# Kernel optimization log

Hardware: AMD Instinct MI355X
Metric: run time of the kernel (lower is better)

The kernel has to match this reference:

```python
import jax, jax.numpy as jnp
import numpy as np
from jax import lax
from jax.scipy.special import logsumexp

N, M, B, T_MAX = 16, 64, 512, 4096


def setup_inputs() -> dict:
    key = jax.random.key(0)
    k1, k2, k3, k4, k5 = jax.random.split(key, 5)
    return {
        "x": jax.random.randint(k1, (B, T_MAX), 0, M),            # observation indices
        "T": jax.random.randint(k2, (B,), 1, T_MAX + 1),          # lengths in [1, T_max]
        "trans_logits": jax.random.normal(k3, (N, N), jnp.float32),
        "emiss_logits": jax.random.normal(k4, (N, M), jnp.float32),
        "prior_logits": jax.random.normal(k5, (N,), jnp.float32),
    }


def reference(x, T, trans_logits, emiss_logits, prior_logits):
    # Normalizations exactly as in the torch module
    log_A = jax.nn.log_softmax(trans_logits, axis=0)   # (N, N), columns normalized: A[i,k] = log p(i | k)
    log_E = jax.nn.log_softmax(emiss_logits, axis=1)   # (N, M)
    log_pi = jax.nn.log_softmax(prior_logits)          # (N,)

    # t = 0: log_alpha[b, i] = log_E[i, x[b,0]] + log_pi[i]
    alpha0 = log_E[:, x[:, 0]].T + log_pi              # (B, N)

    def step(alpha, x_t):
        # new[b, i] = log_E[i, x_t[b]] + logsumexp_k (log_A[i,k] + alpha[b,k])
        trans = logsumexp(log_A[None, :, :] + alpha[:, None, :], axis=2)  # (B, N)
        new = log_E[:, x_t].T + trans
        # carry full alpha; emit only per-step logsumexp to avoid (T,B,N) buffer
        return new, logsumexp(new, axis=1)

    ls0 = logsumexp(alpha0, axis=1)                    # (B,)
    _, ls_rest = lax.scan(step, alpha0, x[:, 1:].T)    # ls_rest: (T_max-1, B)
    log_sums = jnp.concatenate([ls0[None, :], ls_rest], axis=0)  # (T_max, B)

    # gather log p(x_{1..T_b}) at index T_b - 1 for each batch element
    log_probs = jnp.take_along_axis(log_sums.T, (T - 1)[:, None], axis=1)  # (B, 1)
    return jnp.exp(log_probs)


if __name__ == "__main__":
    out = reference(**setup_inputs())
    print(out.shape, out.dtype)
```

## Files before the change

### kernel.cpp

```cpp
#include <hip/hip_runtime.h>
#include <hip/hip_bf16.h>


#define NS    16
#define MOBS  64
#define SSH   5
#define NSEG  32

typedef float f32x4 __attribute__((ext_vector_type(4)));
typedef short s16x4 __attribute__((ext_vector_type(4)));

static __device__ __forceinline__ int imin(int a, int b){ return a < b ? a : b; }

static __device__ __forceinline__ unsigned short f2bf(float f){
  return __bfloat16_as_ushort(__float2bfloat16(f));
}
static __device__ __forceinline__ float b2f(unsigned short u){
  unsigned bits = ((unsigned)u) << 16;
  return __builtin_bit_cast(float, bits);
}

static __device__ __forceinline__ s16x4 pack_bf16x4(f32x4 C){
  unsigned r0, r1;
  asm("v_cvt_pk_bf16_f32 %0, %1, %2" : "=v"(r0) : "v"(C.x), "v"(C.y));
  asm("v_cvt_pk_bf16_f32 %0, %1, %2" : "=v"(r1) : "v"(C.z), "v"(C.w));
  uint2 pu; pu.x = r0; pu.y = r1;
  return __builtin_bit_cast(s16x4, pu);
}

#if __has_builtin(__builtin_amdgcn_mfma_f32_16x16x16bf16_1k)
static __device__ __forceinline__ f32x4 mfma16(s16x4 a, s16x4 b, f32x4 c){
  return __builtin_amdgcn_mfma_f32_16x16x16bf16_1k(a, b, c, 0, 0, 0);
}
#else
static __device__ __forceinline__ f32x4 mfma16(s16x4 a, s16x4 b, f32x4 c){
  f32x4 d;
  asm volatile("v_mfma_f32_16x16x16_bf16 %0, %1, %2, %3"
               : "=&v"(d) : "v"(a), "v"(b), "v"(c));
  return d;
}
#endif


__global__ void hmm_setup(const float* __restrict__ tl, const float* __restrict__ el,
                          const float* __restrict__ pl, float* __restrict__ ws,
                          unsigned short* __restrict__ g2)
{
  int m = blockIdx.x, t = threadIdx.x;
  __shared__ float Al[256];
  __shared__ float ev[16];
  if (t < 16){
    float mx = -3.0e38f;
    for (int i = 0; i < 16; ++i) mx = fmaxf(mx, tl[i*NS + t]);
    float sm = 0.f;
    for (int i = 0; i < 16; ++i) sm += expf(tl[i*NS + t] - mx);
    float inv = 1.f / sm;
    for (int i = 0; i < 16; ++i) Al[i*16 + t] = expf(tl[i*NS + t] - mx) * inv;
  } else if (t < 32){
    int i = t - 16;
    if (m < 64){
      float mx = -3.0e38f;
      for (int mm = 0; mm < MOBS; ++mm) mx = fmaxf(mx, el[i*MOBS + mm]);
      float sm = 0.f;
      for (int mm = 0; mm < MOBS; ++mm) sm += expf(el[i*MOBS + mm] - mx);
      float v = expf(el[i*MOBS + m] - mx) / sm;
      ev[i] = v;
      ws[m*16 + i] = v;
      g2[16640 + m*16 + i] = f2bf(v);
    } else ev[i] = 1.f;
  } else if (t < 48 && m == 64){
    int i = t - 32;
    float mx = -3.0e38f;
    for (int k = 0; k < 16; ++k) mx = fmaxf(mx, pl[k]);
    float sm = 0.f;
    for (int k = 0; k < 16; ++k) sm += expf(pl[k] - mx);
    ws[1024 + i] = expf(pl[i] - mx) / sm;
  }
  __syncthreads();
  int l = t >> 2, e = t & 3;
  int i = l & 15, col = ((l >> 4) << 2) + e;
  float acc;
  if (m == 64){
    acc = Al[i*16 + col];
  } else {
    acc = 0.f;
    #pragma unroll
    for (int k = 0; k < 16; ++k) acc += Al[i*16 + k] * ev[k] * Al[k*16 + col];
  }
  g2[(m*64 + l)*4 + e] = f2bf(acc);
}

template<bool MASK, bool REN>
static __device__ __forceinline__ void run_quad(
    int p0, int npair,
    const unsigned short* g2l, const unsigned short* etl,
    int lane4, int g4, int xp, s16x4& P, int& ce,
    s16x4 (&gf)[4], s16x4 (&ev)[4], s16x4 (&gfn)[4], s16x4 (&evn)[4])
{
  const f32x4 Z = {0.f, 0.f, 0.f, 0.f};
  #pragma unroll
  for (int p = 0; p < 4; ++p){
    int v = __builtin_amdgcn_readlane(xp, (p0 + 4 + p) & 63);
    gfn[p] = *(const s16x4*)&g2l[(v & 63)*256 + lane4];
    evn[p] = *(const s16x4*)&etl[((v >> 8) & 63)*16 + g4];

    f32x4 C = mfma16(gf[p], P, Z);
    C.x *= b2f((unsigned short)ev[p].x);
    C.y *= b2f((unsigned short)ev[p].y);
    C.z *= b2f((unsigned short)ev[p].z);
    C.w *= b2f((unsigned short)ev[p].w);

    bool commit = (!MASK) || (p0 + p < npair);
    if (REN && p == 3){
      float mm = fmaxf(fmaxf(C.x, C.y), fmaxf(C.z, C.w));
      mm = fmaxf(mm, __shfl_xor(mm, 16));
      mm = fmaxf(mm, __shfl_xor(mm, 32));
      int kk; (void)frexpf(mm, &kk);
      if (commit){
        C.x = ldexpf(C.x, -kk); C.y = ldexpf(C.y, -kk);
        C.z = ldexpf(C.z, -kk); C.w = ldexpf(C.w, -kk);
        ce += kk;
      }
    }
    if (commit){
      P = pack_bf16x4(C);
    }
    asm volatile("" ::: "memory");
  }
}

__global__ __launch_bounds__(512, 1) void hmm_seg(
    const int* __restrict__ x, const int* __restrict__ Tl,
    const unsigned short* __restrict__ g2,
    unsigned short* __restrict__ Q, int* __restrict__ CE,
    int TMAX, int XN)
{
  int tid  = threadIdx.x;
  int lane = tid & 63;
  int wid  = __builtin_amdgcn_readfirstlane(tid >> 6);
  int g = lane >> 4, j = lane & 15;
  int lane4 = lane * 4, g4 = g * 4;

  int gseg = blockIdx.x * 8 + wid;
  int b = gseg >> SSH, s = gseg & (NSEG - 1);

  int steps = __builtin_amdgcn_readfirstlane(Tl[b]) - 1;
  int L  = (steps + NSEG - 1) >> SSH;
  int lo = s * L;
  int n  = imin(steps - lo, L);

  unsigned short* Qout = Q + (size_t)gseg * 256;
  int* ceout = CE + gseg * NS;

  int s_lo = (blockIdx.x & 3) * 8;
  if (s_lo * L >= steps){
    if (g == 0) ceout[j] = 0;
    #pragma unroll
    for (int e = 0; e < 4; ++e){
      int k = 4*g + e;
      Qout[k*16 + j] = (k == j) ? (unsigned short)0x3F80 : (unsigned short)0;
    }
    return;
  }

  __shared__ unsigned short g2l[64*256];
  __shared__ unsigned short etl[1024];
  {
    const uint4* s1 = (const uint4*)g2;
    const uint4* s2 = (const uint4*)(g2 + 16640);
    uint4* d1 = (uint4*)g2l;
    uint4* d2 = (uint4*)etl;
    for (int i = tid; i < 2048; i += 512) d1[i] = s1[i];
    if (tid < 128) d2[tid] = s2[tid];
  }
  __syncthreads();

  if (n <= 0){
    if (g == 0) ceout[j] = 0;
    #pragma unroll
    for (int e = 0; e < 4; ++e){
      int k = 4*g + e;
      Qout[k*16 + j] = (k == j) ? (unsigned short)0x3F80 : (unsigned short)0;
    }
    return;
  }

  int npair = n >> 1, odd = n & 1;
  int xbase = b*TMAX + 1 + lo;

  int i0 = xbase + 2*lane;
  int xa = x[imin(i0,     XN - 1)] & 63;
  int xb = x[imin(i0 + 1, XN - 1)] & 63;
  int xp = xa | (xb << 8);

  s16x4 P;
  P.x = (4*g+0 == j) ? (short)0x3F80 : (short)0;
  P.y = (4*g+1 == j) ? (short)0x3F80 : (short)0;
  P.z = (4*g+2 == j) ? (short)0x3F80 : (short)0;
  P.w = (4*g+3 == j) ? (short)0x3F80 : (short)0;

  s16x4 gfA[4], gfB[4], evA[4], evB[4];
  #pragma unroll
  for (int p = 0; p < 4; ++p){
    int v = __builtin_amdgcn_readlane(xp, p);
    gfA[p] = *(const s16x4*)&g2l[(v & 63)*256 + lane4];
    evA[p] = *(const s16x4*)&etl[((v >> 8) & 63)*16 + g4];
  }

  int ce = 0, p0 = 0;
  while (p0 + 8 <= npair){
    run_quad<false,false>(p0,   npair, g2l, etl, lane4, g4, xp, P, ce, gfA, evA, gfB, evB);
    run_quad<false,true >(p0+4, npair, g2l, etl, lane4, g4, xp, P, ce, gfB, evB, gfA, evA);
    p0 += 8;
  }
  if (p0 < npair){
    run_quad<true,true>(p0, npair, g2l, etl, lane4, g4, xp, P, ce, gfA, evA, gfB, evB);
    if (p0 + 4 < npair)
      run_quad<true,true>(p0+4, npair, g2l, etl, lane4, g4, xp, P, ce, gfB, evB, gfA, evA);
  }

  if (odd){
    int v = __builtin_amdgcn_readlane(xp, (n - 1) >> 1);
    int xm = v & 63;
    s16x4 af  = *(const s16x4*)&g2[16384 + lane4];
    s16x4 evo = *(const s16x4*)&etl[xm*16 + g4];
    const f32x4 Z = {0.f,0.f,0.f,0.f};
    f32x4 C = mfma16(af, P, Z);
    C.x *= b2f((unsigned short)evo.x); C.y *= b2f((unsigned short)evo.y);
    C.z *= b2f((unsigned short)evo.z); C.w *= b2f((unsigned short)evo.w);
    P = pack_bf16x4(C);
  }

  if (g == 0) ceout[j] = ce;
  unsigned short pb[4] = {(unsigned short)P.x, (unsigned short)P.y,
                          (unsigned short)P.z, (unsigned short)P.w};
  #pragma unroll
  for (int e = 0; e < 4; ++e) Qout[(4*g + e)*16 + j] = pb[e];
}

__global__ __launch_bounds__(256) void hmm_comb(
    const int* __restrict__ x, const float* __restrict__ ws,
    const unsigned short* __restrict__ Q, const int* __restrict__ CE,
    float* __restrict__ out, int TMAX)
{
  int lane = threadIdx.x & 63;
  int w    = threadIdx.x >> 6;
  int b    = blockIdx.x * 4 + w;
  int k = lane & 15, r = lane >> 4;

  int x0 = x[b*TMAX];
  float u = ws[1024 + k] * ws[x0*16 + k];
  int ce_tot = 0;

  const unsigned short* qb = Q  + (size_t)b * NSEG * 256;
  const int*            cb = CE + b * NSEG * 16;

  s16x4 qq = *(const s16x4*)&qb[k*16 + 4*r];
  int4  cv = *(const int4*)&cb[4*r];

  for (int s = 0; s < NSEG; ++s){
    s16x4 qn; int4 cn;
    if (s + 1 < NSEG){
      qn = *(const s16x4*)&qb[(s+1)*256 + k*16 + 4*r];
      cn = *(const int4*)&cb[(s+1)*16 + 4*r];
    }
    int c0 = __builtin_amdgcn_readlane(cv.x, 0);
    float m0 = ldexpf(b2f((unsigned short)qq.x), cv.x - c0);
    float m1 = ldexpf(b2f((unsigned short)qq.y), cv.y - c0);
    float m2 = ldexpf(b2f((unsigned short)qq.z), cv.z - c0);
    float m3 = ldexpf(b2f((unsigned short)qq.w), cv.w - c0);

    float u0 = __shfl(u, 4*r + 0);
    float u1 = __shfl(u, 4*r + 1);
    float u2 = __shfl(u, 4*r + 2);
    float u3 = __shfl(u, 4*r + 3);
    float acc = m0*u0 + m1*u1 + m2*u2 + m3*u3;
    acc += __shfl_xor(acc, 16);
    acc += __shfl_xor(acc, 32);

    int ek; (void)frexpf(acc, &ek);
    int k0 = __builtin_amdgcn_readlane(ek, 0);
    u = ldexpf(acc, -k0);
    ce_tot += c0 + k0;

    qq = qn; cv = cn;
  }

  float sm = u;
  sm += __shfl_xor(sm, 1);
  sm += __shfl_xor(sm, 2);
  sm += __shfl_xor(sm, 4);
  sm += __shfl_xor(sm, 8);
  if (lane == 0) out[b] = ldexpf(sm, ce_tot);
}

extern "C" void kernel_launch(void* const* d_in, const int* in_sizes, int n_in,
                              void* d_out, int out_size, void* d_ws, size_t ws_size,
                              hipStream_t stream)
{
  (void)n_in; (void)out_size; (void)ws_size;
  const int*   x  = (const int*)  d_in[0];
  const int*   T  = (const int*)  d_in[1];
  const float* tl = (const float*)d_in[2];
  const float* el = (const float*)d_in[3];
  const float* pl = (const float*)d_in[4];
  int B    = in_sizes[1];
  int TMAX = in_sizes[0] / B;
  int XN   = B * TMAX;

  float* ws = (float*)d_ws;
  unsigned short* g2 = (unsigned short*)((char*)d_ws + 8192);
  unsigned short* Q  = (unsigned short*)((char*)d_ws + 49152);
  int* CE = (int*)((char*)d_ws + 49152 + (size_t)B * NSEG * 512);
  float* out = (float*)d_out;

  hipLaunchKernelGGL(hmm_setup, dim3(65),          dim3(256), 0, stream, tl, el, pl, ws, g2);
  hipLaunchKernelGGL(hmm_seg,   dim3(B*NSEG/8),    dim3(512), 0, stream, x, T, g2, Q, CE, TMAX, XN);
  hipLaunchKernelGGL(hmm_comb,  dim3(B/4),         dim3(256), 0, stream, x, ws, Q, CE, out, TMAX);
}
```

Measured before the change: 50.59 us.

## Split each segment into two interleaved MFMA chains and merge via matmul

Each wave now runs two independent matrix-product chains over the two halves of its segment, interleaving their MFMAs so the dependent latency of one chain hides behind the other. The second chain's product is transposed through a small LDS buffer and multiplied onto the first at the end, with one renormalization and a combined exponent. This adds register pressure, an extra LDS round-trip, an extra MFMA per segment, and a change in how bf16 rounding accumulates.

```diff
diff --git a/kernel.cpp b/kernel.cpp
--- a/kernel.cpp
+++ b/kernel.cpp
@@ -91,41 +91,74 @@
 }
 
 template<bool MASK, bool REN>
-static __device__ __forceinline__ void run_quad(
-    int p0, int npair,
+static __device__ __forceinline__ void run_quad2(
+    int p0, int h, int c2n,
     const unsigned short* g2l, const unsigned short* etl,
-    int lane4, int g4, int xp, s16x4& P, int& ce,
-    s16x4 (&gf)[4], s16x4 (&ev)[4], s16x4 (&gfn)[4], s16x4 (&evn)[4])
+    int lane4, int g4, int xp,
+    s16x4& P1, int& ce1,
+    s16x4 (&gf1)[4], s16x4 (&ev1)[4], s16x4 (&g1n)[4], s16x4 (&e1n)[4],
+    s16x4& P2, int& ce2,
+    s16x4 (&gf2)[4], s16x4 (&ev2)[4], s16x4 (&g2n)[4], s16x4 (&e2n)[4])
 {
   const f32x4 Z = {0.f, 0.f, 0.f, 0.f};
   #pragma unroll
   for (int p = 0; p < 4; ++p){
-    int v = __builtin_amdgcn_readlane(xp, (p0 + 4 + p) & 63);
-    gfn[p] = *(const s16x4*)&g2l[(v & 63)*256 + lane4];
-    evn[p] = *(const s16x4*)&etl[((v >> 8) & 63)*16 + g4];
-
-    f32x4 C = mfma16(gf[p], P, Z);
-    C.x *= b2f((unsigned short)ev[p].x);
-    C.y *= b2f((unsigned short)ev[p].y);
-    C.z *= b2f((unsigned short)ev[p].z);
-    C.w *= b2f((unsigned short)ev[p].w);
-
-    bool commit = (!MASK) || (p0 + p < npair);
-    if (REN && p == 3){
-      float mm = fmaxf(fmaxf(C.x, C.y), fmaxf(C.z, C.w));
-      mm = fmaxf(mm, __shfl_xor(mm, 16));
-      mm = fmaxf(mm, __shfl_xor(mm, 32));
-      int kk; (void)frexpf(mm, &kk);
-      if (commit){
-        C.x = ldexpf(C.x, -kk); C.y = ldexpf(C.y, -kk);
-        C.z = ldexpf(C.z, -kk); C.w = ldexpf(C.w, -kk);
-        ce += kk;
+    {
+      int v = __builtin_amdgcn_readlane(xp, (p0 + 4 + p) & 63);
+      g1n[p] = *(const s16x4*)&g2l[(v & 63)*256 + lane4];
+      e1n[p] = *(const s16x4*)&etl[((v >> 8) & 63)*16 + g4];
+
+      f32x4 C = mfma16(gf1[p], P1, Z);
+      C.x *= b2f((unsigned short)ev1[p].x);
+      C.y *= b2f((unsigned short)ev1[p].y);
+      C.z *= b2f((unsigned short)ev1[p].z);
+      C.w *= b2f((unsigned short)ev1[p].w);
+
+      bool commit = (!MASK) || (p0 + p < h);
+      if (REN && p == 3){
+        float mm = fmaxf(fmaxf(C.x, C.y), fmaxf(C.z, C.w));
+        mm = fmaxf(mm, __shfl_xor(mm, 16));
+        mm = fmaxf(mm, __shfl_xor(mm, 32));
+        int kk; (void)frexpf(mm, &kk);
+        if (commit){
+          C.x = ldexpf(C.x, -kk); C.y = ldexpf(C.y, -kk);
+          C.z = ldexpf(C.z, -kk); C.w = ldexpf(C.w, -kk);
+          ce1 += kk;
+        }
       }
-    }
-    if (commit){
-      P = pack_bf16x4(C);
-    }
-    asm volatile("" ::: "memory");
+      if (commit) P1 = pack_bf16x4(C);
+      asm volatile("" ::: "memory");
+    }
+    {
+      int v = __builtin_amdgcn_readlane(xp, (h + p0 + 4 + p) & 63);
+      g2n[p] = *(const s16x4*)&g2l[(v & 63)*256 + lane4];
+      e2n[p] = *(const s16x4*)&etl[((v >> 8) & 63)*16 + g4];
+
+      f32x4 D = mfma16(gf2[p], P2, Z);
+      D.x *= b2f((unsigned short)ev2[p].x);
+      D.y *= b2f((unsigned short)ev2[p].y);
+      D.z *= b2f((unsigned short)ev2[p].z);
+      D.w *= b2f((unsigned short)ev2[p].w);
+
+      bool commit = (!MASK) || (p0 + p < c2n);
+      if (REN && p == 3){
+        float mm = fmaxf(fmaxf(D.x, D.y), fmaxf(D.z, D.w));
+        mm = fmaxf(mm, __shfl_xor(mm, 1));
+        mm = fmaxf(mm, __shfl_xor(mm, 2));
+        mm = fmaxf(mm, __shfl_xor(mm, 4));
+        mm = fmaxf(mm, __shfl_xor(mm, 8));
+        mm = fmaxf(mm, __shfl_xor(mm, 16));
+        mm = fmaxf(mm, __shfl_xor(mm, 32));
+        int kk; (void)frexpf(mm, &kk);
+        if (commit){
+          D.x = ldexpf(D.x, -kk); D.y = ldexpf(D.y, -kk);
+          D.z = ldexpf(D.z, -kk); D.w = ldexpf(D.w, -kk);
+          ce2 += kk;
+        }
+      }
+      if (commit) P2 = pack_bf16x4(D);
+      asm volatile("" ::: "memory");
+    }
   }
 }
 
@@ -165,6 +198,7 @@
 
   __shared__ unsigned short g2l[64*256];
   __shared__ unsigned short etl[1024];
+  __shared__ unsigned short tb[2048];
   {
     const uint4* s1 = (const uint4*)g2;
     const uint4* s2 = (const uint4*)(g2 + 16640);
@@ -186,6 +220,8 @@
   }
 
   int npair = n >> 1, odd = n & 1;
+  int h   = npair >> 1;
+  int c2n = npair - h;
   int xbase = b*TMAX + 1 + lo;
 
   int i0 = xbase + 2*lane;
@@ -193,45 +229,82 @@
   int xb = x[imin(i0 + 1, XN - 1)] & 63;
   int xp = xa | (xb << 8);
 
-  s16x4 P;
-  P.x = (4*g+0 == j) ? (short)0x3F80 : (short)0;
-  P.y = (4*g+1 == j) ? (short)0x3F80 : (short)0;
-  P.z = (4*g+2 == j) ? (short)0x3F80 : (short)0;
-  P.w = (4*g+3 == j) ? (short)0x3F80 : (short)0;
-
-  s16x4 gfA[4], gfB[4], evA[4], evB[4];
+  s16x4 P1, P2;
+  P1.x = (4*g+0 == j) ? (short)0x3F80 : (short)0;
+  P1.y = (4*g+1 == j) ? (short)0x3F80 : (short)0;
+  P1.z = (4*g+2 == j) ? (short)0x3F80 : (short)0;
+  P1.w = (4*g+3 == j) ? (short)0x3F80 : (short)0;
+  P2 = P1;
+
+  s16x4 gf1A[4], gf1B[4], ev1A[4], ev1B[4];
+  s16x4 gf2A[4], gf2B[4], ev2A[4], ev2B[4];
   #pragma unroll
   for (int p = 0; p < 4; ++p){
-    int v = __builtin_amdgcn_readlane(xp, p);
-    gfA[p] = *(const s16x4*)&g2l[(v & 63)*256 + lane4];
-    evA[p] = *(const s16x4*)&etl[((v >> 8) & 63)*16 + g4];
-  }
-
-  int ce = 0, p0 = 0;
-  while (p0 + 8 <= npair){
-    run_quad<false,false>(p0,   npair, g2l, etl, lane4, g4, xp, P, ce, gfA, evA, gfB, evB);
-    run_quad<false,true >(p0+4, npair, g2l, etl, lane4, g4, xp, P, ce, gfB, evB, gfA, evA);
+    int v1 = __builtin_amdgcn_readlane(xp, p);
+    gf1A[p] = *(const s16x4*)&g2l[(v1 & 63)*256 + lane4];
+    ev1A[p] = *(const s16x4*)&etl[((v1 >> 8) & 63)*16 + g4];
+    int v2 = __builtin_amdgcn_readlane(xp, (h + p) & 63);
+    gf2A[p] = *(const s16x4*)&g2l[(v2 & 63)*256 + lane4];
+    ev2A[p] = *(const s16x4*)&etl[((v2 >> 8) & 63)*16 + g4];
+  }
+
+  int ce1 = 0, ce2 = 0, p0 = 0;
+  while (p0 + 8 <= h){
+    run_quad2<false,false>(p0,   h, c2n, g2l, etl, lane4, g4, xp,
+                           P1, ce1, gf1A, ev1A, gf1B, ev1B,
+                           P2, ce2, gf2A, ev2A, gf2B, ev2B);
+    run_quad2<false,true >(p0+4, h, c2n, g2l, etl, lane4, g4, xp,
+                           P1, ce1, gf1B, ev1B, gf1A, ev1A,
+                           P2, ce2, gf2B, ev2B, gf2A, ev2A);
     p0 += 8;
   }
-  if (p0 < npair){
-    run_quad<true,true>(p0, npair, g2l, etl, lane4, g4, xp, P, ce, gfA, evA, gfB, evB);
-    if (p0 + 4 < npair)
-      run_quad<true,true>(p0+4, npair, g2l, etl, lane4, g4, xp, P, ce, gfB, evB, gfA, evA);
-  }
+  if (p0 < c2n){
+    run_quad2<true,true>(p0, h, c2n, g2l, etl, lane4, g4, xp,
+                         P1, ce1, gf1A, ev1A, gf1B, ev1B,
+                         P2, ce2, gf2A, ev2A, gf2B, ev2B);
+    if (p0 + 4 < c2n)
+      run_quad2<true,true>(p0+4, h, c2n, g2l, etl, lane4, g4, xp,
+                           P1, ce1, gf1B, ev1B, gf1A, ev1A,
+                           P2, ce2, gf2B, ev2B, gf2A, ev2A);
+  }
+
+  s16x4 A2;
+  {
+    unsigned short* twave = tb + wid*256;
+    ((uint2*)twave)[lane] = __builtin_bit_cast(uint2, P2);
+    int base = (lane >> 4)*16 + ((lane & 15) >> 2)*64 + (lane & 3);
+    unsigned u0 = twave[base +  0];
+    unsigned u1 = twave[base +  4];
+    unsigned u2 = twave[base +  8];
+    unsigned u3 = twave[base + 12];
+    uint2 au; au.x = u0 | (u1 << 16); au.y = u2 | (u3 << 16);
+    A2 = __builtin_bit_cast(s16x4, au);
+  }
+  const f32x4 Z = {0.f,0.f,0.f,0.f};
+  f32x4 C = mfma16(A2, P1, Z);
+  {
+    float mm = fmaxf(fmaxf(C.x, C.y), fmaxf(C.z, C.w));
+    mm = fmaxf(mm, __shfl_xor(mm, 16));
+    mm = fmaxf(mm, __shfl_xor(mm, 32));
+    int kk; (void)frexpf(mm, &kk);
+    C.x = ldexpf(C.x, -kk); C.y = ldexpf(C.y, -kk);
+    C.z = ldexpf(C.z, -kk); C.w = ldexpf(C.w, -kk);
+    ce1 += ce2 + kk;
+  }
+  s16x4 P = pack_bf16x4(C);
 
   if (odd){
     int v = __builtin_amdgcn_readlane(xp, (n - 1) >> 1);
     int xm = v & 63;
     s16x4 af  = *(const s16x4*)&g2[16384 + lane4];
     s16x4 evo = *(const s16x4*)&etl[xm*16 + g4];
-    const f32x4 Z = {0.f,0.f,0.f,0.f};
-    f32x4 C = mfma16(af, P, Z);
-    C.x *= b2f((unsigned short)evo.x); C.y *= b2f((unsigned short)evo.y);
-    C.z *= b2f((unsigned short)evo.z); C.w *= b2f((unsigned short)evo.w);
-    P = pack_bf16x4(C);
-  }
-
-  if (g == 0) ceout[j] = ce;
+    f32x4 Co = mfma16(af, P, Z);
+    Co.x *= b2f((unsigned short)evo.x); Co.y *= b2f((unsigned short)evo.y);
+    Co.z *= b2f((unsigned short)evo.z); Co.w *= b2f((unsigned short)evo.w);
+    P = pack_bf16x4(Co);
+  }
+
+  if (g == 0) ceout[j] = ce1;
   unsigned short pb[4] = {(unsigned short)P.x, (unsigned short)P.y,
                           (unsigned short)P.z, (unsigned short)P.w};
   #pragma unroll
```

Result: slower. 57.03 us (+12.7%).

## Fuse segment-combine into segment kernel via last-block atomic counter

Applied to the files above, without the earlier changes.

Removes the separate combine kernel launch. Each of the 4 blocks serving a batch element bumps an atomic counter after finishing its segments, and the last block's first wave runs the sequential 32-segment combine and writes the output. The setup kernel zeroes the counters. This saves a launch and its gap, but adds threadfences, an atomic and a block-wide sync, and the combine now runs in a single wave inside the tail blocks.

```diff
diff --git a/kernel.cpp b/kernel.cpp
--- a/kernel.cpp
+++ b/kernel.cpp
@@ -44,11 +44,15 @@
 
 __global__ void hmm_setup(const float* __restrict__ tl, const float* __restrict__ el,
                           const float* __restrict__ pl, float* __restrict__ ws,
-                          unsigned short* __restrict__ g2)
+                          unsigned short* __restrict__ g2, int* __restrict__ cnt,
+                          int B)
 {
   int m = blockIdx.x, t = threadIdx.x;
   __shared__ float Al[256];
   __shared__ float ev[16];
+  if (m == 64){
+    for (int i = t; i < B; i += 256) cnt[i] = 0;
+  }
   if (t < 16){
     float mx = -3.0e38f;
     for (int i = 0; i < 16; ++i) mx = fmaxf(mx, tl[i*NS + t]);
@@ -131,10 +135,15 @@
 
 __global__ __launch_bounds__(512, 1) void hmm_seg(
     const int* __restrict__ x, const int* __restrict__ Tl,
+    const float* __restrict__ wsf,
     const unsigned short* __restrict__ g2,
     unsigned short* __restrict__ Q, int* __restrict__ CE,
+    int* __restrict__ cnt, float* __restrict__ out,
     int TMAX, int XN)
 {
+  __shared__ unsigned short g2l[64*256];
+  __shared__ unsigned short etl[1024];
+
   int tid  = threadIdx.x;
   int lane = tid & 63;
   int wid  = __builtin_amdgcn_readfirstlane(tid >> 6);
@@ -153,145 +162,145 @@
   int* ceout = CE + gseg * NS;
 
   int s_lo = (blockIdx.x & 3) * 8;
-  if (s_lo * L >= steps){
+  bool blk_empty = (s_lo * L >= steps);
+
+  if (blk_empty){
     if (g == 0) ceout[j] = 0;
     #pragma unroll
     for (int e = 0; e < 4; ++e){
       int k = 4*g + e;
       Qout[k*16 + j] = (k == j) ? (unsigned short)0x3F80 : (unsigned short)0;
     }
-    return;
-  }
-
-  __shared__ unsigned short g2l[64*256];
-  __shared__ unsigned short etl[1024];
-  {
-    const uint4* s1 = (const uint4*)g2;
-    const uint4* s2 = (const uint4*)(g2 + 16640);
-    uint4* d1 = (uint4*)g2l;
-    uint4* d2 = (uint4*)etl;
-    for (int i = tid; i < 2048; i += 512) d1[i] = s1[i];
-    if (tid < 128) d2[tid] = s2[tid];
-  }
+  } else {
+    {
+      const uint4* s1 = (const uint4*)g2;
+      const uint4* s2 = (const uint4*)(g2 + 16640);
+      uint4* d1 = (uint4*)g2l;
+      uint4* d2 = (uint4*)etl;
+      for (int i = tid; i < 2048; i += 512) d1[i] = s1[i];
+      if (tid < 128) d2[tid] = s2[tid];
+    }
+    __syncthreads();
+
+    if (n <= 0){
+      if (g == 0) ceout[j] = 0;
+      #pragma unroll
+      for (int e = 0; e < 4; ++e){
+        int k = 4*g + e;
+        Qout[k*16 + j] = (k == j) ? (unsigned short)0x3F80 : (unsigned short)0;
+      }
+    } else {
+      int npair = n >> 1, odd = n & 1;
+      int xbase = b*TMAX + 1 + lo;
+
+      int i0 = xbase + 2*lane;
+      int xa = x[imin(i0,     XN - 1)] & 63;
+      int xb = x[imin(i0 + 1, XN - 1)] & 63;
+      int xp = xa | (xb << 8);
+
+      s16x4 P;
+      P.x = (4*g+0 == j) ? (short)0x3F80 : (short)0;
+      P.y = (4*g+1 == j) ? (short)0x3F80 : (short)0;
+      P.z = (4*g+2 == j) ? (short)0x3F80 : (short)0;
+      P.w = (4*g+3 == j) ? (short)0x3F80 : (short)0;
+
+      s16x4 gfA[4], gfB[4], evA[4], evB[4];
+      #pragma unroll
+      for (int p = 0; p < 4; ++p){
+        int v = __builtin_amdgcn_readlane(xp, p);
+        gfA[p] = *(const s16x4*)&g2l[(v & 63)*256 + lane4];
+        evA[p] = *(const s16x4*)&etl[((v >> 8) & 63)*16 + g4];
+      }
+
+      int ce = 0, p0 = 0;
+      while (p0 + 8 <= npair){
+        run_quad<false,false>(p0,   npair, g2l, etl, lane4, g4, xp, P, ce, gfA, evA, gfB, evB);
+        run_quad<false,true >(p0+4, npair, g2l, etl, lane4, g4, xp, P, ce, gfB, evB, gfA, evA);
+        p0 += 8;
+      }
+      if (p0 < npair){
+        run_quad<true,true>(p0, npair, g2l, etl, lane4, g4, xp, P, ce, gfA, evA, gfB, evB);
+        if (p0 + 4 < npair)
+          run_quad<true,true>(p0+4, npair, g2l, etl, lane4, g4, xp, P, ce, gfB, evB, gfA, evA);
+      }
+
+      if (odd){
+        int v = __builtin_amdgcn_readlane(xp, (n - 1) >> 1);
+        int xm = v & 63;
+        s16x4 af  = *(const s16x4*)&g2[16384 + lane4];
+        s16x4 evo = *(const s16x4*)&etl[xm*16 + g4];
+        const f32x4 Z = {0.f,0.f,0.f,0.f};
+        f32x4 C = mfma16(af, P, Z);
+        C.x *= b2f((unsigned short)evo.x); C.y *= b2f((unsigned short)evo.y);
+        C.z *= b2f((unsigned short)evo.z); C.w *= b2f((unsigned short)evo.w);
+        P = pack_bf16x4(C);
+      }
+
+      if (g == 0) ceout[j] = ce;
+      unsigned short pb[4] = {(unsigned short)P.x, (unsigned short)P.y,
+                              (unsigned short)P.z, (unsigned short)P.w};
+      #pragma unroll
+      for (int e = 0; e < 4; ++e) Qout[(4*g + e)*16 + j] = pb[e];
+    }
+  }
+
   __syncthreads();
-
-  if (n <= 0){
-    if (g == 0) ceout[j] = 0;
-    #pragma unroll
-    for (int e = 0; e < 4; ++e){
-      int k = 4*g + e;
-      Qout[k*16 + j] = (k == j) ? (unsigned short)0x3F80 : (unsigned short)0;
-    }
-    return;
-  }
-
-  int npair = n >> 1, odd = n & 1;
-  int xbase = b*TMAX + 1 + lo;
-
-  int i0 = xbase + 2*lane;
-  int xa = x[imin(i0,     XN - 1)] & 63;
-  int xb = x[imin(i0 + 1, XN - 1)] & 63;
-  int xp = xa | (xb << 8);
-
-  s16x4 P;
-  P.x = (4*g+0 == j) ? (short)0x3F80 : (short)0;
-  P.y = (4*g+1 == j) ? (short)0x3F80 : (short)0;
-  P.z = (4*g+2 == j) ? (short)0x3F80 : (short)0;
-  P.w = (4*g+3 == j) ? (short)0x3F80 : (short)0;
-
-  s16x4 gfA[4], gfB[4], evA[4], evB[4];
-  #pragma unroll
-  for (int p = 0; p < 4; ++p){
-    int v = __builtin_amdgcn_readlane(xp, p);
-    gfA[p] = *(const s16x4*)&g2l[(v & 63)*256 + lane4];
-    evA[p] = *(const s16x4*)&etl[((v >> 8) & 63)*16 + g4];
-  }
-
-  int ce = 0, p0 = 0;
-  while (p0 + 8 <= npair){
-    run_quad<false,false>(p0,   npair, g2l, etl, lane4, g4, xp, P, ce, gfA, evA, gfB, evB);
-    run_quad<false,true >(p0+4, npair, g2l, etl, lane4, g4, xp, P, ce, gfB, evB, gfA, evA);
-    p0 += 8;
-  }
-  if (p0 < npair){
-    run_quad<true,true>(p0, npair, g2l, etl, lane4, g4, xp, P, ce, gfA, evA, gfB, evB);
-    if (p0 + 4 < npair)
-      run_quad<true,true>(p0+4, npair, g2l, etl, lane4, g4, xp, P, ce, gfB, evB, gfA, evA);
-  }
-
-  if (odd){
-    int v = __builtin_amdgcn_readlane(xp, (n - 1) >> 1);
-    int xm = v & 63;
-    s16x4 af  = *(const s16x4*)&g2[16384 + lane4];
-    s16x4 evo = *(const s16x4*)&etl[xm*16 + g4];
-    const f32x4 Z = {0.f,0.f,0.f,0.f};
-    f32x4 C = mfma16(af, P, Z);
-    C.x *= b2f((unsigned short)evo.x); C.y *= b2f((unsigned short)evo.y);
-    C.z *= b2f((unsigned short)evo.z); C.w *= b2f((unsigned short)evo.w);
-    P = pack_bf16x4(C);
-  }
-
-  if (g == 0) ceout[j] = ce;
-  unsigned short pb[4] = {(unsigned short)P.x, (unsigned short)P.y,
-                          (unsigned short)P.z, (unsigned short)P.w};
-  #pragma unroll
-  for (int e = 0; e < 4; ++e) Qout[(4*g + e)*16 + j] = pb[e];
-}
-
-__global__ __launch_bounds__(256) void hmm_comb(
-    const int* __restrict__ x, const float* __restrict__ ws,
-    const unsigned short* __restrict__ Q, const int* __restrict__ CE,
-    float* __restrict__ out, int TMAX)
-{
-  int lane = threadIdx.x & 63;
-  int w    = threadIdx.x >> 6;
-  int b    = blockIdx.x * 4 + w;
-  int k = lane & 15, r = lane >> 4;
-
-  int x0 = x[b*TMAX];
-  float u = ws[1024 + k] * ws[x0*16 + k];
-  int ce_tot = 0;
-
-  const unsigned short* qb = Q  + (size_t)b * NSEG * 256;
-  const int*            cb = CE + b * NSEG * 16;
-
-  s16x4 qq = *(const s16x4*)&qb[k*16 + 4*r];
-  int4  cv = *(const int4*)&cb[4*r];
-
-  for (int s = 0; s < NSEG; ++s){
-    s16x4 qn; int4 cn;
-    if (s + 1 < NSEG){
-      qn = *(const s16x4*)&qb[(s+1)*256 + k*16 + 4*r];
-      cn = *(const int4*)&cb[(s+1)*16 + 4*r];
-    }
-    int c0 = __builtin_amdgcn_readlane(cv.x, 0);
-    float m0 = ldexpf(b2f((unsigned short)qq.x), cv.x - c0);
-    float m1 = ldexpf(b2f((unsigned short)qq.y), cv.y - c0);
-    float m2 = ldexpf(b2f((unsigned short)qq.z), cv.z - c0);
-    float m3 = ldexpf(b2f((unsigned short)qq.w), cv.w - c0);
-
-    float u0 = __shfl(u, 4*r + 0);
-    float u1 = __shfl(u, 4*r + 1);
-    float u2 = __shfl(u, 4*r + 2);
-    float u3 = __shfl(u, 4*r + 3);
-    float acc = m0*u0 + m1*u1 + m2*u2 + m3*u3;
-    acc += __shfl_xor(acc, 16);
-    acc += __shfl_xor(acc, 32);
-
-    int ek; (void)frexpf(acc, &ek);
-    int k0 = __builtin_amdgcn_readlane(ek, 0);
-    u = ldexpf(acc, -k0);
-    ce_tot += c0 + k0;
-
-    qq = qn; cv = cn;
-  }
-
-  float sm = u;
-  sm += __shfl_xor(sm, 1);
-  sm += __shfl_xor(sm, 2);
-  sm += __shfl_xor(sm, 4);
-  sm += __shfl_xor(sm, 8);
-  if (lane == 0) out[b] = ldexpf(sm, ce_tot);
+  if (wid == 0){
+    int old = 0;
+    if (lane == 0){
+      __threadfence();
+      old = atomicAdd(&cnt[b], 1);
+    }
+    old = __shfl(old, 0);
+    if (old == 3){
+      __threadfence();
+      int k = lane & 15, r = lane >> 4;
+      int x0 = x[b*TMAX];
+      float u = wsf[1024 + k] * wsf[x0*16 + k];
+      int ce_tot = 0;
+
+      const unsigned short* qb2 = Q  + (size_t)b * NSEG * 256;
+      const int*            cb2 = CE + b * NSEG * 16;
+
+      s16x4 qq = *(const s16x4*)&qb2[k*16 + 4*r];
+      int4  cv = *(const int4*)&cb2[4*r];
+
+      for (int s2 = 0; s2 < NSEG; ++s2){
+        s16x4 qn; int4 cn;
+        if (s2 + 1 < NSEG){
+          qn = *(const s16x4*)&qb2[(s2+1)*256 + k*16 + 4*r];
+          cn = *(const int4*)&cb2[(s2+1)*16 + 4*r];
+        }
+        int c0 = __builtin_amdgcn_readlane(cv.x, 0);
+        float m0 = ldexpf(b2f((unsigned short)qq.x), cv.x - c0);
+        float m1 = ldexpf(b2f((unsigned short)qq.y), cv.y - c0);
+        float m2 = ldexpf(b2f((unsigned short)qq.z), cv.z - c0);
+        float m3 = ldexpf(b2f((unsigned short)qq.w), cv.w - c0);
+
+        float u0 = __shfl(u, 4*r + 0);
+        float u1 = __shfl(u, 4*r + 1);
+        float u2 = __shfl(u, 4*r + 2);
+        float u3 = __shfl(u, 4*r + 3);
+        float acc = m0*u0 + m1*u1 + m2*u2 + m3*u3;
+        acc += __shfl_xor(acc, 16);
+        acc += __shfl_xor(acc, 32);
+
+        int ek; (void)frexpf(acc, &ek);
+        int k0 = __builtin_amdgcn_readlane(ek, 0);
+        u = ldexpf(acc, -k0);
+        ce_tot += c0 + k0;
+
+        qq = qn; cv = cn;
+      }
+
+      float sm = u;
+      sm += __shfl_xor(sm, 1);
+      sm += __shfl_xor(sm, 2);
+      sm += __shfl_xor(sm, 4);
+      sm += __shfl_xor(sm, 8);
+      if (lane == 0) out[b] = ldexpf(sm, ce_tot);
+    }
+  }
 }
 
 extern "C" void kernel_launch(void* const* d_in, const int* in_sizes, int n_in,
@@ -309,12 +318,12 @@
   int XN   = B * TMAX;
 
   float* ws = (float*)d_ws;
+  int* cnt = (int*)((char*)d_ws + 6144);
   unsigned short* g2 = (unsigned short*)((char*)d_ws + 8192);
   unsigned short* Q  = (unsigned short*)((char*)d_ws + 49152);
   int* CE = (int*)((char*)d_ws + 49152 + (size_t)B * NSEG * 512);
   float* out = (float*)d_out;
 
-  hipLaunchKernelGGL(hmm_setup, dim3(65),          dim3(256), 0, stream, tl, el, pl, ws, g2);
-  hipLaunchKernelGGL(hmm_seg,   dim3(B*NSEG/8),    dim3(512), 0, stream, x, T, g2, Q, CE, TMAX, XN);
-  hipLaunchKernelGGL(hmm_comb,  dim3(B/4),         dim3(256), 0, stream, x, ws, Q, CE, out, TMAX);
-}
+  hipLaunchKernelGGL(hmm_setup, dim3(65),          dim3(256), 0, stream, tl, el, pl, ws, g2, cnt, B);
+  hipLaunchKernelGGL(hmm_seg,   dim3(B*NSEG/8),    dim3(512), 0, stream, x, T, ws, g2, Q, CE, cnt, out, TMAX, XN);
+}
```

Result: slower. 139.4 us (+175.7%).
